# Kernel tuning notes

Measured on AMD Instinct MI355X. Metric: run time of the kernel, lower is better.

Reference implementation:

```python
import jax, jax.numpy as jnp
import numpy as np

EMBED_DIM = 1024
FFN_DIM = 4096
N_QUBITS = 10


def setup_inputs() -> dict:
    key = jax.random.key(0)
    k_x, k_phi, k_w1, k_w2 = jax.random.split(key, 4)
    x = jax.random.normal(k_x, (8, 2048, EMBED_DIM), dtype=jnp.float32)
    # trainable RY angles, one per wire (torchquantum init ~ U(0, 2pi); any init works for a reference)
    ry_params = jax.random.uniform(k_phi, (N_QUBITS,), dtype=jnp.float32, minval=0.0, maxval=2.0 * np.pi)
    # nn.Linear(n_qubits, ffn_dim, bias=False): weight [ffn_dim, n_qubits]
    w1 = jax.random.normal(k_w1, (FFN_DIM, N_QUBITS), dtype=jnp.float32) / np.sqrt(N_QUBITS)
    # nn.Linear(ffn_dim, embed_dim, bias=False): weight [embed_dim, ffn_dim]
    w2 = jax.random.normal(k_w2, (EMBED_DIM, FFN_DIM), dtype=jnp.float32) / np.sqrt(FFN_DIM)
    return {"x": x, "ry_params": ry_params, "w1": w1, "w2": w2}


def reference(x, ry_params, w1, w2):
    # Quantum layer in closed form: wires are unentangled.
    # |0> --RX(x_i)--RY(phi_i)--> <Z_i> = cos(x_i) * cos(phi_i)
    # Only the first N_QUBITS features of each token are encoded.
    q_out = jnp.cos(x[..., :N_QUBITS]) * jnp.cos(ry_params)  # [B, S, nq]
    # dropout is identity in eval mode
    h = jnp.einsum('bsq,fq->bsf', q_out, w1)  # [B, S, ffn]
    h = jax.nn.relu(h)
    return jnp.einsum('bsf,ef->bse', h, w2)  # [B, S, embed]
```

## Files before the change

kernel.cpp:

```cpp
#include <hip/hip_runtime.h>
#include <stdint.h>

#define M_TOK   16384
#define EMBED   1024
#define FFN     4096
#define NQ      10

#define GK 4096
#define GN 1024
#define BK 64
#define NT (GK / BK)

typedef __attribute__((ext_vector_type(8))) short  bf16x8;
typedef __attribute__((ext_vector_type(4))) float  f32x4;
typedef __attribute__((ext_vector_type(8))) unsigned short u16x8;

static __device__ __forceinline__ unsigned short f2bf(float f) {
    union { float f; unsigned u; } v; v.f = f;
    unsigned r = v.u + 0x7FFF + ((v.u >> 16) & 1);
    return (unsigned short)(r >> 16);
}

__global__ __launch_bounds__(256) void prep_w1(
    const float* __restrict__ w1, const float* __restrict__ ry,
    float* __restrict__ w1cT)
{
    __shared__ float cry[16];
    if (threadIdx.x < NQ) cry[threadIdx.x] = cosf(ry[threadIdx.x]);
    __syncthreads();
    const int f = blockIdx.x * 256 + threadIdx.x;
#pragma unroll
    for (int i = 0; i < NQ; ++i)
        w1cT[i * FFN + f] = w1[f * NQ + i] * cry[i];
}

__global__ __launch_bounds__(256) void compute_h(
    const float* __restrict__ x, const float* __restrict__ w1cT,
    unsigned short* __restrict__ h)
{
    __shared__ float cq[32 * 16];

    const int tid = threadIdx.x;
    const int t0  = blockIdx.x * 32;
    const int fb  = blockIdx.y * 2048 + tid * 8;

    for (int idx = tid; idx < 32 * NQ; idx += 256) {
        int t = idx / NQ;
        int i = idx - t * NQ;
        cq[t * 16 + i] = cosf(x[(size_t)(t0 + t) * EMBED + i]);
    }
    __syncthreads();

    float wf[8][NQ];
#pragma unroll
    for (int i = 0; i < NQ; ++i) {
        const float4 lo = *(const float4*)(w1cT + (size_t)i * FFN + fb);
        const float4 hi = *(const float4*)(w1cT + (size_t)i * FFN + fb + 4);
        wf[0][i] = lo.x; wf[1][i] = lo.y; wf[2][i] = lo.z; wf[3][i] = lo.w;
        wf[4][i] = hi.x; wf[5][i] = hi.y; wf[6][i] = hi.z; wf[7][i] = hi.w;
    }

    for (int t = 0; t < 32; ++t) {
        const float4 c0 = *(const float4*)&cq[t * 16 + 0];
        const float4 c1 = *(const float4*)&cq[t * 16 + 4];
        const float2 c2 = *(const float2*)&cq[t * 16 + 8];
        u16x8 v;
#pragma unroll
        for (int fi = 0; fi < 8; ++fi) {
            float s = c0.x * wf[fi][0] + c0.y * wf[fi][1] + c0.z * wf[fi][2]
                    + c0.w * wf[fi][3] + c1.x * wf[fi][4] + c1.y * wf[fi][5]
                    + c1.z * wf[fi][6] + c1.w * wf[fi][7] + c2.x * wf[fi][8]
                    + c2.y * wf[fi][9];
            v[fi] = f2bf(fmaxf(s, 0.f));
        }
        *(u16x8*)(h + (size_t)(t0 + t) * FFN + fb) = v;
    }
}

__global__ __launch_bounds__(256) void conv_w2(
    const float* __restrict__ w2, unsigned short* __restrict__ o)
{
    const int idx = (blockIdx.x * 256 + threadIdx.x) * 8;
    float4 a = *(const float4*)(w2 + idx);
    float4 b = *(const float4*)(w2 + idx + 4);
    u16x8 v;
    v[0] = f2bf(a.x); v[1] = f2bf(a.y); v[2] = f2bf(a.z); v[3] = f2bf(a.w);
    v[4] = f2bf(b.x); v[5] = f2bf(b.y); v[6] = f2bf(b.z); v[7] = f2bf(b.w);
    *(u16x8*)(o + idx) = v;
}

#define GL2LDS(g, l) \
    __builtin_amdgcn_global_load_lds( \
        (const __attribute__((address_space(1))) void*)(g), \
        (__attribute__((address_space(3))) void*)(l), 16, 0, 0)

__global__ __launch_bounds__(512, 2) void gemm_bt(
    const unsigned short* __restrict__ A,
    const unsigned short* __restrict__ B,
    float* __restrict__ C)
{
    __shared__ __align__(16) unsigned short As[2][256 * BK];
    __shared__ __align__(16) unsigned short Bs[2][256 * BK];

    const int tid  = threadIdx.x;
    const int wv   = tid >> 6;
    const int lane = tid & 63;
    const int wm   = wv >> 2;
    const int wn   = wv & 3;

    const int bid = blockIdx.x;
    const int wg  = (bid & 7) * 32 + (bid >> 3);
    const int m0  = (wg >> 2) * 256;
    const int n0  = (wg & 3) * 256;

    const int srow8 = lane >> 3;
    const int schk  = (lane & 7) ^ srow8;
    const char* ag = (const char*)A +
        ((size_t)(m0 + wv * 16 + srow8) * GK + schk * 8) * 2;
    const char* bg = (const char*)B +
        ((size_t)(n0 + wv * 16 + srow8) * GK + schk * 8) * 2;
    const size_t ROW8 = (size_t)8 * GK * 2;
    const size_t HALF = (size_t)128 * GK * 2;

#define STAGE_A(buf, half, ko) do { \
    GL2LDS(ag + (ko) + (half) * HALF,        (char*)As[buf] + ((half) * 128 + wv * 16) * 128); \
    GL2LDS(ag + (ko) + (half) * HALF + ROW8, (char*)As[buf] + ((half) * 128 + wv * 16 + 8) * 128); \
} while (0)
#define STAGE_B(buf, half, ko) do { \
    GL2LDS(bg + (ko) + (half) * HALF,        (char*)Bs[buf] + ((half) * 128 + wv * 16) * 128); \
    GL2LDS(bg + (ko) + (half) * HALF + ROW8, (char*)Bs[buf] + ((half) * 128 + wv * 16 + 8) * 128); \
} while (0)

    const int rr  = lane & 15;
    const int fsw = lane & 7;
    const int cc  = lane >> 4;
#define CHOFF(s) ((((s) * 4 + cc) ^ fsw) * 16)
#define RD_A(dst, Pt, mh) do { \
    _Pragma("unroll") \
    for (int s_ = 0; s_ < 2; ++s_) \
        _Pragma("unroll") \
        for (int i_ = 0; i_ < 4; ++i_) \
            dst[s_][i_] = *(const bf16x8*)((Pt) + \
                ((mh) * 128 + wm * 64 + i_ * 16 + rr) * 128 + CHOFF(s_)); \
} while (0)
#define RD_B(dst, Pt, nh) do { \
    _Pragma("unroll") \
    for (int s_ = 0; s_ < 2; ++s_) \
        _Pragma("unroll") \
        for (int j_ = 0; j_ < 2; ++j_) \
            dst[s_][j_] = *(const bf16x8*)((Pt) + \
                ((nh) * 128 + wn * 32 + j_ * 16 + rr) * 128 + CHOFF(s_)); \
} while (0)

    f32x4 acc[8][4] = {};

#define MFMA16(AF, BF, I0, J0) do { \
    __builtin_amdgcn_s_setprio(1); \
    _Pragma("unroll") \
    for (int s_ = 0; s_ < 2; ++s_) \
        _Pragma("unroll") \
        for (int i_ = 0; i_ < 4; ++i_) \
            _Pragma("unroll") \
            for (int j_ = 0; j_ < 2; ++j_) \
                acc[(I0) + i_][(J0) + j_] = __builtin_amdgcn_mfma_f32_16x16x32_bf16( \
                    AF[s_][i_], BF[s_][j_], acc[(I0) + i_][(J0) + j_], 0, 0, 0); \
    __builtin_amdgcn_s_setprio(0); \
} while (0)

#define SYNC_IN do { \
    __builtin_amdgcn_s_barrier(); \
    asm volatile("s_waitcnt lgkmcnt(0)" ::: "memory"); \
    __builtin_amdgcn_sched_barrier(0); \
} while (0)
#define SYNC_OUT do { \
    asm volatile("s_waitcnt vmcnt(4)" ::: "memory"); \
    __builtin_amdgcn_s_barrier(); \
} while (0)

    bf16x8 aF[2][4], b0[2][2], b1[2][2];

    STAGE_A(0, 0, 0); STAGE_B(0, 0, 0);
    STAGE_B(0, 1, 0); STAGE_A(0, 1, 0);
    asm volatile("s_waitcnt vmcnt(4)" ::: "memory");
    __builtin_amdgcn_s_barrier();

#define TILE4(cur, SH1, SH2, SH3, SH4) do { \
    const char* At = (const char*)As[cur]; \
    const char* Bt = (const char*)Bs[cur]; \
     \
    RD_A(aF, At, 0); RD_B(b0, Bt, 0); \
    SH1; \
    SYNC_IN; MFMA16(aF, b0, 0, 0); SYNC_OUT; \
     \
    RD_B(b1, Bt, 1); \
    SH2; \
    SYNC_IN; MFMA16(aF, b1, 0, 2); SYNC_OUT; \
     \
    RD_A(aF, At, 1); \
    SH3; \
    SYNC_IN; MFMA16(aF, b1, 4, 2); SYNC_OUT; \
     \
    SH4; \
    SYNC_IN; MFMA16(aF, b0, 4, 0); SYNC_OUT; \
} while (0)

#pragma unroll 1
    for (int tt = 0; tt < NT / 2; ++tt) {
        const size_t kv = (size_t)(2 * tt + 1) * 128;
        const size_t ku = (2 * tt + 2 < NT) ? (size_t)(2 * tt + 2) * 128 : 0;
        TILE4(0, STAGE_A(1, 0, kv), STAGE_B(1, 0, kv),
                 STAGE_B(1, 1, kv), STAGE_A(1, 1, kv));
        TILE4(1, STAGE_A(0, 0, ku), STAGE_B(0, 0, ku),
                 STAGE_B(0, 1, ku), STAGE_A(0, 1, ku));
    }

    asm volatile("s_waitcnt vmcnt(0)" ::: "memory");

    const int cn = lane & 15;
    const int rb = (lane >> 4) * 4;
#pragma unroll
    for (int i = 0; i < 8; ++i)
#pragma unroll
        for (int j = 0; j < 4; ++j)
#pragma unroll
            for (int r = 0; r < 4; ++r) {
                const int m = m0 + (i >> 2) * 128 + wm * 64 + (i & 3) * 16 + rb + r;
                const int n = n0 + (j >> 1) * 128 + wn * 32 + (j & 1) * 16 + cn;
                C[(size_t)m * GN + n] = acc[i][j][r];
            }
}

extern "C" void kernel_launch(void* const* d_in, const int* in_sizes, int n_in,
                              void* d_out, int out_size, void* d_ws, size_t ws_size,
                              hipStream_t stream) {
    const float* x  = (const float*)d_in[0];
    const float* ry = (const float*)d_in[1];
    const float* w1 = (const float*)d_in[2];
    const float* w2 = (const float*)d_in[3];
    float* out = (float*)d_out;

    unsigned short* h   = (unsigned short*)d_ws;
    unsigned short* w2b = (unsigned short*)((char*)d_ws +
                           (size_t)M_TOK * FFN * sizeof(unsigned short));
    float* w1cT = (float*)w2b;

    prep_w1<<<dim3(FFN / 256), 256, 0, stream>>>(w1, ry, w1cT);
    compute_h<<<dim3(512, 2), 256, 0, stream>>>(x, w1cT, h);
    conv_w2<<<dim3((EMBED * FFN) / (256 * 8)), 256, 0, stream>>>(w2, w2b);
    gemm_bt<<<dim3(256), 512, 0, stream>>>(h, w2b, out);
}
```

Measured before the change: 280.8 us.

## Deepen GEMM prefetch pipeline by staging next tile's quarters earlier

Restructures the bf16 GEMM main loop so most of the following K-tile is already in flight before the current tile is consumed. Each half-buffer is refilled as soon as its last reader finishes, with explicit vmcnt(6) and lgkmcnt(8) waits and fewer barrier/waitcnt pairs per sub-step. The aim is to hide global-to-LDS latency behind MFMA work. The trade-off is more loads in flight and waits hand-tuned to an exact count of outstanding operations, which can introduce LDS read/write races if any count is wrong.

```diff
diff --git a/kernel.cpp b/kernel.cpp
--- a/kernel.cpp
+++ b/kernel.cpp
@@ -167,51 +167,78 @@
     __builtin_amdgcn_s_setprio(0); \
 } while (0)
 
-#define SYNC_IN do { \
-    __builtin_amdgcn_s_barrier(); \
-    asm volatile("s_waitcnt lgkmcnt(0)" ::: "memory"); \
-    __builtin_amdgcn_sched_barrier(0); \
-} while (0)
-#define SYNC_OUT do { \
-    asm volatile("s_waitcnt vmcnt(4)" ::: "memory"); \
-    __builtin_amdgcn_s_barrier(); \
-} while (0)
+#define BAR      __builtin_amdgcn_s_barrier()
+#define LGKM0    asm volatile("s_waitcnt lgkmcnt(0)" ::: "memory")
+#define LGKM8    asm volatile("s_waitcnt lgkmcnt(8)" ::: "memory")
+#define VM6      asm volatile("s_waitcnt vmcnt(6)" ::: "memory")
 
     bf16x8 aF[2][4], b0[2][2], b1[2][2];
 
-    STAGE_A(0, 0, 0); STAGE_B(0, 0, 0);
-    STAGE_B(0, 1, 0); STAGE_A(0, 1, 0);
-    asm volatile("s_waitcnt vmcnt(4)" ::: "memory");
-    __builtin_amdgcn_s_barrier();
-
-#define TILE4(cur, SH1, SH2, SH3, SH4) do { \
-    const char* At = (const char*)As[cur]; \
-    const char* Bt = (const char*)Bs[cur]; \
-     \
-    RD_A(aF, At, 0); RD_B(b0, Bt, 0); \
-    SH1; \
-    SYNC_IN; MFMA16(aF, b0, 0, 0); SYNC_OUT; \
-     \
-    RD_B(b1, Bt, 1); \
-    SH2; \
-    SYNC_IN; MFMA16(aF, b1, 0, 2); SYNC_OUT; \
-     \
-    RD_A(aF, At, 1); \
-    SH3; \
-    SYNC_IN; MFMA16(aF, b1, 4, 2); SYNC_OUT; \
-     \
-    SH4; \
-    SYNC_IN; MFMA16(aF, b0, 4, 0); SYNC_OUT; \
-} while (0)
+    STAGE_A(0, 0, 0);   STAGE_B(0, 0, 0);
+    STAGE_B(0, 1, 0);   STAGE_A(0, 1, 0);
+    STAGE_A(1, 0, 128); STAGE_B(1, 0, 128); STAGE_B(1, 1, 128);
+    VM6;
+    BAR;
 
 #pragma unroll 1
     for (int tt = 0; tt < NT / 2; ++tt) {
+        const char* A0p = (const char*)As[0];
+        const char* B0p = (const char*)Bs[0];
+        const char* A1p = (const char*)As[1];
+        const char* B1p = (const char*)Bs[1];
         const size_t kv = (size_t)(2 * tt + 1) * 128;
-        const size_t ku = (2 * tt + 2 < NT) ? (size_t)(2 * tt + 2) * 128 : 0;
-        TILE4(0, STAGE_A(1, 0, kv), STAGE_B(1, 0, kv),
-                 STAGE_B(1, 1, kv), STAGE_A(1, 1, kv));
-        TILE4(1, STAGE_A(0, 0, ku), STAGE_B(0, 0, ku),
-                 STAGE_B(0, 1, ku), STAGE_A(0, 1, ku));
+        const size_t k2 = (2 * tt + 2 < NT) ? (size_t)(2 * tt + 2) * 128 : 0;
+        const size_t k3 = (2 * tt + 3 < NT) ? (size_t)(2 * tt + 3) * 128 : 0;
+
+        RD_A(aF, A0p, 0); RD_B(b0, B0p, 0);
+        STAGE_A(1, 1, kv);
+        LGKM8;
+        BAR; LGKM0;
+        MFMA16(aF, b0, 0, 0);
+        BAR;
+
+        RD_B(b1, B0p, 1);
+        STAGE_A(0, 0, k2);
+        BAR; LGKM0;
+        MFMA16(aF, b1, 0, 2);
+        BAR;
+
+        RD_A(aF, A0p, 1);
+        STAGE_B(0, 0, k2);
+        BAR; LGKM0;
+        MFMA16(aF, b1, 4, 2);
+        BAR;
+
+        STAGE_B(0, 1, k2);
+        BAR;
+        MFMA16(aF, b0, 4, 0);
+        VM6;
+        BAR;
+
+        RD_A(aF, A1p, 0); RD_B(b0, B1p, 0);
+        STAGE_A(0, 1, k2);
+        LGKM8;
+        BAR; LGKM0;
+        MFMA16(aF, b0, 0, 0);
+        BAR;
+
+        RD_B(b1, B1p, 1);
+        STAGE_A(1, 0, k3);
+        BAR; LGKM0;
+        MFMA16(aF, b1, 0, 2);
+        BAR;
+
+        RD_A(aF, A1p, 1);
+        STAGE_B(1, 0, k3);
+        BAR; LGKM0;
+        MFMA16(aF, b1, 4, 2);
+        BAR;
+
+        STAGE_B(1, 1, k3);
+        BAR;
+        MFMA16(aF, b0, 4, 0);
+        VM6;
+        BAR;
     }
 
     asm volatile("s_waitcnt vmcnt(0)" ::: "memory");
```

Result: no change. 280.1 us (-0.2%).
